# Kernel optimization log

Measured on AMD Instinct MI355X. Metric: run time of the kernel, lower is better.

Reference implementation:

```python
import jax, jax.numpy as jnp
import numpy as np

B, C, H, W = 8, 192, 128, 128
NH = 4  # num_heads
EPS = 1e-12


def setup_inputs() -> dict:
    key = jax.random.key(0)
    ks = jax.random.split(key, 10)
    s = 1.0 / np.sqrt(C)
    return {
        "x_q": jax.random.normal(ks[0], (B, C, H, W), jnp.float32),
        "x_k": jax.random.normal(ks[1], (B, C, H, W), jnp.float32),
        "Wq": jax.random.uniform(ks[2], (C, C), jnp.float32, -s, s),
        "bq": jax.random.uniform(ks[3], (C,), jnp.float32, -s, s),
        "Wkv": jax.random.uniform(ks[4], (2 * C, C), jnp.float32, -s, s),
        "bkv": jax.random.uniform(ks[5], (2 * C,), jnp.float32, -s, s),
        "Wp": jax.random.uniform(ks[6], (C, C), jnp.float32, -s, s),
        "bp": jax.random.uniform(ks[7], (C,), jnp.float32, -s, s),
        "temperature": jnp.ones((NH, 1, 1), jnp.float32),
    }


def _l2norm(x, axis):
    # torch F.normalize: x / clamp_min(||x||, eps)
    n = jnp.sqrt(jnp.sum(x * x, axis=axis, keepdims=True))
    return x / jnp.maximum(n, EPS)


def reference(x_q, x_k, Wq, bq, Wkv, bkv, Wp, bp, temperature):
    # 1x1 convs == channel matmuls
    q = jnp.einsum('oc,bchw->bohw', Wq, x_q) + bq[:, None, None]
    kv = jnp.einsum('oc,bchw->bohw', Wkv, x_k) + bkv[:, None, None]
    k, v = jnp.split(kv, 2, axis=1)

    def heads(t):  # (B,C,H,W) -> (B,NH,C//NH, H*W)
        return t.reshape(B, NH, C // NH, H * W)

    q, k, v = heads(q), heads(k), heads(v)
    q = _l2norm(q, 2)
    k = _l2norm(k, 2)

    attn_scale = 0.1 * jax.nn.sigmoid(temperature)  # (NH,1,1)
    attn = jnp.einsum('bhcd,bhkd->bhck', q, k) * attn_scale
    attn = jax.nn.softmax(attn, axis=-1)
    out = jnp.einsum('bhck,bhkd->bhcd', attn, v)
    out = out.reshape(B, C, H, W)
    out = jnp.einsum('oc,bchw->bohw', Wp, out) + bp[:, None, None]
    return out
```

## Files before the change

### kernel.cpp

```cpp
#include <hip/hip_runtime.h>
#include <hip/hip_bf16.h>

#define HW 16384
#define CC 192
#define BB 8
#define NHD 4
#define HD 48

typedef __attribute__((ext_vector_type(8))) short  short8;
typedef __attribute__((ext_vector_type(4))) float  f32x4;

static __device__ __forceinline__ unsigned short f2bf(float f) {
  unsigned u = __float_as_uint(f);
  u += 0x7fffu + ((u >> 16) & 1u);
  return (unsigned short)(u >> 16);
}
static __device__ __forceinline__ unsigned pk2bf(float lo, float hi) {
  __hip_bfloat162 h = __float22bfloat162_rn(make_float2(lo, hi));
  return *reinterpret_cast<unsigned*>(&h);
}

static __device__ __forceinline__ void ldsbar() {
  asm volatile("" ::: "memory");
  asm volatile("s_waitcnt lgkmcnt(0)" ::: "memory");
  __builtin_amdgcn_s_barrier();
  asm volatile("" ::: "memory");
}

#define SWZ_COL(row, cdw) ((cdw) ^ ((((row) >> 3) & 3) << 2))

__global__ __launch_bounds__(256) void cast_w_kernel(
    const float* __restrict__ Wq, const float* __restrict__ Wkv,
    unsigned short* __restrict__ Wb)
{
  const int i = blockIdx.x * 256 + threadIdx.x;
  const float v = (i < CC*CC) ? Wq[i] : Wkv[i - CC*CC];
  Wb[i] = f2bf(v);
}

__global__ __launch_bounds__(512, 2) void qkg_kernel(
    const float* __restrict__ x_q, const float* __restrict__ x_k,
    const unsigned short* __restrict__ wb,
    const float* __restrict__ bq, const float* __restrict__ bkv,
    float* __restrict__ gpart)
{
  const int tid  = threadIdx.x;
  const int lane = tid & 63;
  const int wv   = tid >> 6;
  const int half = wv >> 2;
  const int hh   = wv & 3;
  const int b    = blockIdx.y;
  const int p0   = blockIdx.x * 512;
  const int l15  = lane & 15;
  const int lg   = lane >> 4;
  const int ht   = tid & 255;
  const int qd   = ht & 15;

  __shared__ unsigned short Xsq[64][200];
  __shared__ unsigned short Xsk[64][200];
  __shared__ unsigned short QN[NHD][48][68];
  __shared__ unsigned short KN[NHD][48][68];

  const float* Xsrc = (half ? x_k : x_q) + (size_t)b*CC*HW;
  unsigned short (*Xdst)[200] = half ? Xsk : Xsq;
  unsigned short (*DST)[68]   = half ? KN[hh] : QN[hh];

  const unsigned short* W = wb + (size_t)half*CC*CC;
  short8 afr[6][3];
  #pragma unroll
  for (int kk = 0; kk < 6; ++kk)
    #pragma unroll
    for (int mt = 0; mt < 3; ++mt)
      afr[kk][mt] = *(const short8*)(W + (size_t)(hh*48 + mt*16 + l15)*CC + kk*32 + lg*8);

  const float* bias = half ? bkv : bq;
  float bv[3][4];
  #pragma unroll
  for (int mt = 0; mt < 3; ++mt)
    #pragma unroll
    for (int r = 0; r < 4; ++r)
      bv[mt][r] = bias[hh*48 + mt*16 + lg*4 + r];

  f32x4 pre[12];
  auto LOADT = [&](int pb) {
    #pragma unroll
    for (int i = 0; i < 6; ++i) {
      const int cp = (ht >> 4) + i*16;
      const float* base = Xsrc + (size_t)(2*cp)*HW + pb + qd*4;
      pre[2*i]   = *(const f32x4*)(base);
      pre[2*i+1] = *(const f32x4*)(base + HW);
    }
  };
  auto WRITET = [&]() {
    #pragma unroll
    for (int i = 0; i < 6; ++i) {
      const int cp = (ht >> 4) + i*16;
      #pragma unroll
      for (int j = 0; j < 4; ++j) {
        const int row = qd*4 + j;
        *(unsigned*)&Xdst[row][2*SWZ_COL(row, cp)] =
            pk2bf(pre[2*i][j], pre[2*i+1][j]);
      }
    }
  };

  f32x4 gacc[3][3];
  #pragma unroll
  for (int mt = 0; mt < 3; ++mt)
    #pragma unroll
    for (int nt = 0; nt < 3; ++nt)
      gacc[mt][nt] = (f32x4){0.f, 0.f, 0.f, 0.f};

  LOADT(p0);
  for (int t = 0; t < 8; ++t) {
    WRITET();
    ldsbar();
    if (t < 7) LOADT(p0 + (t+1)*64);

    f32x4 acc[3][4];
    #pragma unroll
    for (int mt = 0; mt < 3; ++mt)
      #pragma unroll
      for (int nt = 0; nt < 4; ++nt)
        acc[mt][nt] = (f32x4){0.f, 0.f, 0.f, 0.f};

    #pragma unroll
    for (int kk = 0; kk < 6; ++kk) {
      short8 bfr[4];
      #pragma unroll
      for (int nt = 0; nt < 4; ++nt) {
        const int lgs = lg ^ ((2*nt + (l15 >> 3)) & 3);
        bfr[nt] = *(const short8*)&Xdst[nt*16 + l15][kk*32 + lgs*8];
      }
      #pragma unroll
      for (int mt = 0; mt < 3; ++mt)
        #pragma unroll
        for (int nt = 0; nt < 4; ++nt)
          acc[mt][nt] = __builtin_amdgcn_mfma_f32_16x16x32_bf16(
              afr[kk][mt], bfr[nt], acc[mt][nt], 0, 0, 0);
    }

    #pragma unroll
    for (int nt = 0; nt < 4; ++nt) {
      float v[3][4];
      float ss = 0.f;
      #pragma unroll
      for (int mt = 0; mt < 3; ++mt)
        #pragma unroll
        for (int r = 0; r < 4; ++r) {
          const float x = acc[mt][nt][r] + bv[mt][r];
          v[mt][r] = x;
          ss += x*x;
        }
      ss += __shfl_xor(ss, 16);
      ss += __shfl_xor(ss, 32);
      const float rn = 1.0f / fmaxf(sqrtf(ss), 1e-12f);
      #pragma unroll
      for (int mt = 0; mt < 3; ++mt)
        #pragma unroll
        for (int r = 0; r < 4; ++r)
          DST[mt*16 + lg*4 + r][nt*16 + l15] = f2bf(v[mt][r] * rn);
    }
    ldsbar();

    {
      const int s = half;
      short8 ga[3], gb[3];
      #pragma unroll
      for (int mt = 0; mt < 3; ++mt)
        ga[mt] = *(const short8*)&QN[hh][mt*16 + l15][s*32 + lg*8];
      #pragma unroll
      for (int nt = 0; nt < 3; ++nt)
        gb[nt] = *(const short8*)&KN[hh][nt*16 + l15][s*32 + lg*8];
      #pragma unroll
      for (int mt = 0; mt < 3; ++mt)
        #pragma unroll
        for (int nt = 0; nt < 3; ++nt)
          gacc[mt][nt] = __builtin_amdgcn_mfma_f32_16x16x32_bf16(
              ga[mt], gb[nt], gacc[mt][nt], 0, 0, 0);
    }
  }

  float* G = gpart + ((size_t)(b*NHD + hh)*64 + blockIdx.x*2 + half)*2304;
  #pragma unroll
  for (int mt = 0; mt < 3; ++mt)
    #pragma unroll
    for (int nt = 0; nt < 3; ++nt)
      #pragma unroll
      for (int r = 0; r < 4; ++r)
        G[(mt*16 + lg*4 + r)*HD + nt*16 + l15] = gacc[mt][nt][r];
}

__global__ __launch_bounds__(256) void proj_fin(
    const float* __restrict__ x_k,
    const unsigned short* __restrict__ w3b,
    const float* __restrict__ b3,
    float* __restrict__ of)
{
  const int tid  = threadIdx.x;
  const int lane = tid & 63;
  const int wv   = tid >> 6;
  const int b    = blockIdx.y;
  const int p0   = blockIdx.x * 256;
  const int l15  = lane & 15;
  const int lg   = lane >> 4;
  const int qd   = tid & 15;

  __shared__ unsigned short Xt[2][64][200];

  const float* X = x_k + (size_t)b*CC*HW;
  const unsigned short* Wb = w3b + (size_t)b*CC*CC;
  const float* bias = b3 + (size_t)b*CC;

  short8 afr[6][3];
  #pragma unroll
  for (int kk = 0; kk < 6; ++kk)
    #pragma unroll
    for (int mt = 0; mt < 3; ++mt)
      afr[kk][mt] = *(const short8*)(Wb + (size_t)(wv*48 + mt*16 + l15)*CC + kk*32 + lg*8);

  float bv[3][4];
  #pragma unroll
  for (int mt = 0; mt < 3; ++mt)
    #pragma unroll
    for (int r = 0; r < 4; ++r)
      bv[mt][r] = bias[wv*48 + mt*16 + lg*4 + r];

  f32x4 pre[12];
  auto LOADT = [&](int pb) {
    #pragma unroll
    for (int i = 0; i < 6; ++i) {
      const int cp = (tid >> 4) + i*16;
      const float* base = X + (size_t)(2*cp)*HW + pb + qd*4;
      pre[2*i]   = *(const f32x4*)(base);
      pre[2*i+1] = *(const f32x4*)(base + HW);
    }
  };
  auto WRITET = [&](int buf) {
    #pragma unroll
    for (int i = 0; i < 6; ++i) {
      const int cp = (tid >> 4) + i*16;
      #pragma unroll
      for (int j = 0; j < 4; ++j) {
        const int row = qd*4 + j;
        *(unsigned*)&Xt[buf][row][2*SWZ_COL(row, cp)] =
            pk2bf(pre[2*i][j], pre[2*i+1][j]);
      }
    }
  };

  float* Ofp = of + (size_t)b*CC*HW;

  auto COMPUTE = [&](int buf, int pb) {
    f32x4 acc[3][4];
    #pragma unroll
    for (int mt = 0; mt < 3; ++mt)
      #pragma unroll
      for (int nt = 0; nt < 4; ++nt)
        acc[mt][nt] = (f32x4){0.f, 0.f, 0.f, 0.f};

    #pragma unroll
    for (int kk = 0; kk < 6; ++kk) {
      short8 bfr[4];
      #pragma unroll
      for (int nt = 0; nt < 4; ++nt) {
        const int lgs = lg ^ ((2*nt + (l15 >> 3)) & 3);
        bfr[nt] = *(const short8*)&Xt[buf][nt*16 + l15][kk*32 + lgs*8];
      }
      #pragma unroll
      for (int mt = 0; mt < 3; ++mt)
        #pragma unroll
        for (int nt = 0; nt < 4; ++nt)
          acc[mt][nt] = __builtin_amdgcn_mfma_f32_16x16x32_bf16(
              afr[kk][mt], bfr[nt], acc[mt][nt], 0, 0, 0);
    }

    #pragma unroll
    for (int nt = 0; nt < 4; ++nt) {
      const int col = pb + nt*16 + l15;
      #pragma unroll
      for (int mt = 0; mt < 3; ++mt)
        #pragma unroll
        for (int r = 0; r < 4; ++r)
          Ofp[(size_t)(wv*48 + mt*16 + lg*4 + r)*HW + col] = acc[mt][nt][r] + bv[mt][r];
    }
  };

  LOADT(p0);
  WRITET(0);
  ldsbar();
  #pragma unroll
  for (int t = 0; t < 4; ++t) {
    if (t < 3) LOADT(p0 + (t+1)*64);
    COMPUTE(t & 1, p0 + t*64);
    if (t < 3) {
      WRITET((t & 1) ^ 1);
      ldsbar();
    }
  }
}

__global__ __launch_bounds__(256) void attn_m_kernel(
    const float* __restrict__ Gpart,
    const float* __restrict__ Wp,
    const float* __restrict__ temp,
    float* __restrict__ Mf)
{
  __shared__ float att[HD][52];
  const int bh  = blockIdx.x;
  const int b   = bh >> 2, h = bh & 3;
  const int tid = threadIdx.x;
  const float* src = Gpart + (size_t)bh*64*2304;

  #pragma unroll
  for (int i = 0; i < 9; ++i) {
    const int e = tid + i*256;
    float s = 0.f;
    #pragma unroll
    for (int k = 0; k < 64; ++k) s += src[(size_t)k*2304 + e];
    att[e/48][e%48] = s;
  }
  __syncthreads();

  const int g = tid >> 2, sl = tid & 3;
  if (g < HD) {
    const float t = temp[h];
    const float scale = 0.1f / (1.0f + expf(-t));
    float* row = att[g];
    float m = -1e30f;
    #pragma unroll
    for (int jj = 0; jj < 12; ++jj) m = fmaxf(m, row[sl + jj*4]);
    m = fmaxf(m, __shfl_xor(m, 1));
    m = fmaxf(m, __shfl_xor(m, 2));
    float ev[12];
    float s = 0.f;
    #pragma unroll
    for (int jj = 0; jj < 12; ++jj) {
      const float e = expf((row[sl + jj*4] - m) * scale);
      ev[jj] = e; s += e;
    }
    s += __shfl_xor(s, 1);
    s += __shfl_xor(s, 2);
    const float inv = 1.0f / s;
    #pragma unroll
    for (int jj = 0; jj < 12; ++jj) row[sl + jj*4] = ev[jj] * inv;
  }
  __syncthreads();

  #pragma unroll
  for (int i = 0; i < 36; ++i) {
    const int idx = tid + i*256;
    const int o = idx / HD, k2 = idx % HD;
    const float* wrow = Wp + (size_t)o*CC + h*HD;
    float s = 0.f;
    #pragma unroll
    for (int c = 0; c < HD; ++c) s += wrow[c] * att[c][k2];
    Mf[(size_t)b*CC*CC + (size_t)o*CC + h*HD + k2] = s;
  }
}

__global__ __launch_bounds__(192) void w3_kernel(
    const float* __restrict__ Mf, const float* __restrict__ Wkv,
    const float* __restrict__ bkv, const float* __restrict__ bp,
    unsigned short* __restrict__ W3b, float* __restrict__ b3)
{
  const int b  = blockIdx.x;
  const int o0 = blockIdx.y * 8;
  const int j  = threadIdx.x;
  const float* M  = Mf + ((size_t)b*CC + o0)*CC;
  const float* Wv = Wkv + (size_t)CC*CC;
  const float* bv = bkv + CC;

  float acc[8]  = {0.f,0.f,0.f,0.f,0.f,0.f,0.f,0.f};
  float bacc[8] = {0.f,0.f,0.f,0.f,0.f,0.f,0.f,0.f};
  #pragma unroll 4
  for (int k = 0; k < CC; ++k) {
    const float w  = Wv[(size_t)k*CC + j];
    const float bk = bv[k];
    #pragma unroll
    for (int r = 0; r < 8; ++r) {
      const float m = M[r*CC + k];
      acc[r]  += m * w;
      bacc[r] += m * bk;
    }
  }
  unsigned short* dst = W3b + ((size_t)b*CC + o0)*CC + j;
  #pragma unroll
  for (int r = 0; r < 8; ++r) dst[(size_t)r*CC] = f2bf(acc[r]);
  if (j < 8) b3[(size_t)b*CC + o0 + j] = bacc[j] + bp[o0 + j];
}

extern "C" void kernel_launch(void* const* d_in, const int* in_sizes, int n_in,
                              void* d_out, int out_size, void* d_ws, size_t ws_size,
                              hipStream_t stream)
{
  (void)in_sizes; (void)n_in; (void)out_size; (void)ws_size;
  const float* x_q  = (const float*)d_in[0];
  const float* x_k  = (const float*)d_in[1];
  const float* Wq   = (const float*)d_in[2];
  const float* bq   = (const float*)d_in[3];
  const float* Wkv  = (const float*)d_in[4];
  const float* bkv  = (const float*)d_in[5];
  const float* Wp   = (const float*)d_in[6];
  const float* bp   = (const float*)d_in[7];
  const float* temp = (const float*)d_in[8];

  char* p = (char*)d_ws;
  float* gpart = (float*)p;                 p += (size_t)BB*NHD*64*2304*sizeof(float);
  float* mf = (float*)p;                    p += (size_t)BB*CC*CC*sizeof(float);
  unsigned short* w3b = (unsigned short*)p; p += (size_t)BB*CC*CC*sizeof(unsigned short);
  float* b3 = (float*)p;                    p += (size_t)BB*CC*sizeof(float);
  unsigned short* wb = (unsigned short*)p;

  cast_w_kernel<<<dim3((2*CC*CC)/256), 256, 0, stream>>>(Wq, Wkv, wb);

  qkg_kernel<<<dim3(HW/512, BB), 512, 0, stream>>>(
      x_q, x_k, wb, bq, bkv, gpart);

  attn_m_kernel<<<dim3(BB*NHD), 256, 0, stream>>>(gpart, Wp, temp, mf);
  w3_kernel<<<dim3(BB, 24), 192, 0, stream>>>(mf, Wkv, bkv, bp, w3b, b3);

  proj_fin<<<dim3(HW/256, BB), 256, 0, stream>>>(x_k, w3b, b3, (float*)d_out);
}
```

Baseline: 173.2 us.

## Alias normalized Q/K tiles onto X staging LDS and stream weight fragments

In the QK Gram kernel, the normalized Q/K tiles now reuse the X staging buffers instead of separate shared arrays, which lowers LDS per block. An extra barrier is added before the overwrite and at the end of each iteration to keep the aliasing safe. Both kernels now reload weight fragments from global memory per k-step instead of holding all 18 fragments in registers, and proj_fin gets a launch bound of 3 blocks per CU. The aim is higher occupancy from fewer registers and less LDS, at the cost of repeated weight loads and more synchronization.

```diff
diff --git a/kernel.cpp b/kernel.cpp
--- a/kernel.cpp
+++ b/kernel.cpp
@@ -56,23 +56,16 @@
   const int ht   = tid & 255;
   const int qd   = ht & 15;
 
-  __shared__ unsigned short Xsq[64][200];
-  __shared__ unsigned short Xsk[64][200];
-  __shared__ unsigned short QN[NHD][48][68];
-  __shared__ unsigned short KN[NHD][48][68];
+  __shared__ unsigned short LDS0[64][200];
+  __shared__ unsigned short LDS1[64][200];
+  unsigned short* QNb = &LDS0[0][0];
+  unsigned short* KNb = &LDS1[0][0];
 
   const float* Xsrc = (half ? x_k : x_q) + (size_t)b*CC*HW;
-  unsigned short (*Xdst)[200] = half ? Xsk : Xsq;
-  unsigned short (*DST)[68]   = half ? KN[hh] : QN[hh];
+  unsigned short (*Xdst)[200] = half ? LDS1 : LDS0;
+  unsigned short* DSTb = (half ? KNb : QNb) + hh*48*66;
 
   const unsigned short* W = wb + (size_t)half*CC*CC;
-  short8 afr[6][3];
-  #pragma unroll
-  for (int kk = 0; kk < 6; ++kk)
-    #pragma unroll
-    for (int mt = 0; mt < 3; ++mt)
-      afr[kk][mt] = *(const short8*)(W + (size_t)(hh*48 + mt*16 + l15)*CC + kk*32 + lg*8);
-
   const float* bias = half ? bkv : bq;
   float bv[3][4];
   #pragma unroll
@@ -126,7 +119,10 @@
 
     #pragma unroll
     for (int kk = 0; kk < 6; ++kk) {
-      short8 bfr[4];
+      short8 afr[3], bfr[4];
+      #pragma unroll
+      for (int mt = 0; mt < 3; ++mt)
+        afr[mt] = *(const short8*)(W + (size_t)(hh*48 + mt*16 + l15)*CC + kk*32 + lg*8);
       #pragma unroll
       for (int nt = 0; nt < 4; ++nt) {
         const int lgs = lg ^ ((2*nt + (l15 >> 3)) & 3);
@@ -137,19 +133,18 @@
         #pragma unroll
         for (int nt = 0; nt < 4; ++nt)
           acc[mt][nt] = __builtin_amdgcn_mfma_f32_16x16x32_bf16(
-              afr[kk][mt], bfr[nt], acc[mt][nt], 0, 0, 0);
+              afr[mt], bfr[nt], acc[mt][nt], 0, 0, 0);
     }
 
     #pragma unroll
     for (int nt = 0; nt < 4; ++nt) {
-      float v[3][4];
       float ss = 0.f;
       #pragma unroll
       for (int mt = 0; mt < 3; ++mt)
         #pragma unroll
         for (int r = 0; r < 4; ++r) {
           const float x = acc[mt][nt][r] + bv[mt][r];
-          v[mt][r] = x;
+          acc[mt][nt][r] = x;
           ss += x*x;
         }
       ss += __shfl_xor(ss, 16);
@@ -159,8 +154,17 @@
       for (int mt = 0; mt < 3; ++mt)
         #pragma unroll
         for (int r = 0; r < 4; ++r)
-          DST[mt*16 + lg*4 + r][nt*16 + l15] = f2bf(v[mt][r] * rn);
-    }
+          acc[mt][nt][r] *= rn;
+    }
+    ldsbar();
+
+    #pragma unroll
+    for (int nt = 0; nt < 4; ++nt)
+      #pragma unroll
+      for (int mt = 0; mt < 3; ++mt)
+        #pragma unroll
+        for (int r = 0; r < 4; ++r)
+          DSTb[(mt*16 + lg*4 + r)*66 + nt*16 + l15] = f2bf(acc[mt][nt][r]);
     ldsbar();
 
     {
@@ -168,10 +172,10 @@
       short8 ga[3], gb[3];
       #pragma unroll
       for (int mt = 0; mt < 3; ++mt)
-        ga[mt] = *(const short8*)&QN[hh][mt*16 + l15][s*32 + lg*8];
+        ga[mt] = *(const short8*)(QNb + hh*48*66 + (mt*16 + l15)*66 + s*32 + lg*8);
       #pragma unroll
       for (int nt = 0; nt < 3; ++nt)
-        gb[nt] = *(const short8*)&KN[hh][nt*16 + l15][s*32 + lg*8];
+        gb[nt] = *(const short8*)(KNb + hh*48*66 + (nt*16 + l15)*66 + s*32 + lg*8);
       #pragma unroll
       for (int mt = 0; mt < 3; ++mt)
         #pragma unroll
@@ -179,6 +183,7 @@
           gacc[mt][nt] = __builtin_amdgcn_mfma_f32_16x16x32_bf16(
               ga[mt], gb[nt], gacc[mt][nt], 0, 0, 0);
     }
+    ldsbar();
   }
 
   float* G = gpart + ((size_t)(b*NHD + hh)*64 + blockIdx.x*2 + half)*2304;
@@ -191,7 +196,7 @@
         G[(mt*16 + lg*4 + r)*HD + nt*16 + l15] = gacc[mt][nt][r];
 }
 
-__global__ __launch_bounds__(256) void proj_fin(
+__global__ __launch_bounds__(256, 3) void proj_fin(
     const float* __restrict__ x_k,
     const unsigned short* __restrict__ w3b,
     const float* __restrict__ b3,
@@ -212,13 +217,6 @@
   const unsigned short* Wb = w3b + (size_t)b*CC*CC;
   const float* bias = b3 + (size_t)b*CC;
 
-  short8 afr[6][3];
-  #pragma unroll
-  for (int kk = 0; kk < 6; ++kk)
-    #pragma unroll
-    for (int mt = 0; mt < 3; ++mt)
-      afr[kk][mt] = *(const short8*)(Wb + (size_t)(wv*48 + mt*16 + l15)*CC + kk*32 + lg*8);
-
   float bv[3][4];
   #pragma unroll
   for (int mt = 0; mt < 3; ++mt)
@@ -261,7 +259,10 @@
 
     #pragma unroll
     for (int kk = 0; kk < 6; ++kk) {
-      short8 bfr[4];
+      short8 afr[3], bfr[4];
+      #pragma unroll
+      for (int mt = 0; mt < 3; ++mt)
+        afr[mt] = *(const short8*)(Wb + (size_t)(wv*48 + mt*16 + l15)*CC + kk*32 + lg*8);
       #pragma unroll
       for (int nt = 0; nt < 4; ++nt) {
         const int lgs = lg ^ ((2*nt + (l15 >> 3)) & 3);
@@ -272,7 +273,7 @@
         #pragma unroll
         for (int nt = 0; nt < 4; ++nt)
           acc[mt][nt] = __builtin_amdgcn_mfma_f32_16x16x32_bf16(
-              afr[kk][mt], bfr[nt], acc[mt][nt], 0, 0, 0);
+              afr[mt], bfr[nt], acc[mt][nt], 0, 0, 0);
     }
 
     #pragma unroll
```

After: 212.2 us. 22.5% more time.

## Load 128-pixel rows per wave, write LDS in alternating halves, reload weights per k-step

Applied to the files above, without the earlier changes.

The X-tile global loads are reorganized so each wave reads 48 channels across 128 contiguous pixels, refilling every other iteration. Half the lanes write their 64-pixel slice to LDS on alternate iterations, using a new XOR swizzle and 16-bit scattered stores. The weight A-fragments are no longer kept resident in registers and are reloaded from global/L2 for each k-step. This frees registers and lengthens contiguous global reads, at the cost of repeated weight loads, narrower LDS stores and possible bank conflicts.

```diff
diff --git a/kernel.cpp b/kernel.cpp
--- a/kernel.cpp
+++ b/kernel.cpp
@@ -27,6 +27,8 @@
   asm volatile("" ::: "memory");
 }
 
+#define SWZ3(rowq) ((((rowq) & 7)) << 3)
+
 #define SWZ_COL(row, cdw) ((cdw) ^ ((((row) >> 3) & 3) << 2))
 
 __global__ __launch_bounds__(256) void cast_w_kernel(
@@ -49,12 +51,13 @@
   const int wv   = tid >> 6;
   const int half = wv >> 2;
   const int hh   = wv & 3;
+  const int wq   = wv & 3;
   const int b    = blockIdx.y;
   const int p0   = blockIdx.x * 512;
   const int l15  = lane & 15;
   const int lg   = lane >> 4;
-  const int ht   = tid & 255;
-  const int qd   = ht & 15;
+  const int ch2  = lane >> 5;
+  const int pl32 = lane & 31;
 
   __shared__ unsigned short Xsq[64][200];
   __shared__ unsigned short Xsk[64][200];
@@ -66,13 +69,6 @@
   unsigned short (*DST)[68]   = half ? KN[hh] : QN[hh];
 
   const unsigned short* W = wb + (size_t)half*CC*CC;
-  short8 afr[6][3];
-  #pragma unroll
-  for (int kk = 0; kk < 6; ++kk)
-    #pragma unroll
-    for (int mt = 0; mt < 3; ++mt)
-      afr[kk][mt] = *(const short8*)(W + (size_t)(hh*48 + mt*16 + l15)*CC + kk*32 + lg*8);
-
   const float* bias = half ? bkv : bq;
   float bv[3][4];
   #pragma unroll
@@ -81,25 +77,27 @@
     for (int r = 0; r < 4; ++r)
       bv[mt][r] = bias[hh*48 + mt*16 + lg*4 + r];
 
-  f32x4 pre[12];
-  auto LOADT = [&](int pb) {
-    #pragma unroll
-    for (int i = 0; i < 6; ++i) {
-      const int cp = (ht >> 4) + i*16;
-      const float* base = Xsrc + (size_t)(2*cp)*HW + pb + qd*4;
-      pre[2*i]   = *(const f32x4*)(base);
-      pre[2*i+1] = *(const f32x4*)(base + HW);
+  f32x4 pre[24];
+  auto LOADT = [&](int pbase) {
+    #pragma unroll
+    for (int i = 0; i < 24; ++i) {
+      const int c = wq*48 + 2*i + ch2;
+      pre[i] = *(const f32x4*)(Xsrc + (size_t)c*HW + pbase + pl32*4);
     }
   };
-  auto WRITET = [&]() {
-    #pragma unroll
-    for (int i = 0; i < 6; ++i) {
-      const int cp = (ht >> 4) + i*16;
-      #pragma unroll
-      for (int j = 0; j < 4; ++j) {
-        const int row = qd*4 + j;
-        *(unsigned*)&Xdst[row][2*SWZ_COL(row, cp)] =
-            pk2bf(pre[2*i][j], pre[2*i+1][j]);
+  auto WRITET = [&](int sel) {
+    if ((pl32 >> 4) == sel) {
+      const int pq = pl32 & 15;
+      #pragma unroll
+      for (int i = 0; i < 24; ++i) {
+        const int c  = wq*48 + 2*i + ch2;
+        const int cs = c ^ SWZ3(pq);
+        const unsigned u0 = pk2bf(pre[i][0], pre[i][1]);
+        const unsigned u1 = pk2bf(pre[i][2], pre[i][3]);
+        Xdst[pq*4 + 0][cs] = (unsigned short)u0;
+        Xdst[pq*4 + 1][cs] = (unsigned short)(u0 >> 16);
+        Xdst[pq*4 + 2][cs] = (unsigned short)u1;
+        Xdst[pq*4 + 3][cs] = (unsigned short)(u1 >> 16);
       }
     }
   };
@@ -113,9 +111,9 @@
 
   LOADT(p0);
   for (int t = 0; t < 8; ++t) {
-    WRITET();
+    WRITET(t & 1);
     ldsbar();
-    if (t < 7) LOADT(p0 + (t+1)*64);
+    if ((t & 1) && t < 7) LOADT(p0 + (t+1)*64);
 
     f32x4 acc[3][4];
     #pragma unroll
@@ -126,18 +124,21 @@
 
     #pragma unroll
     for (int kk = 0; kk < 6; ++kk) {
-      short8 bfr[4];
+      short8 afr[3], bfr[4];
+      #pragma unroll
+      for (int mt = 0; mt < 3; ++mt)
+        afr[mt] = *(const short8*)(W + (size_t)(hh*48 + mt*16 + l15)*CC + kk*32 + lg*8);
       #pragma unroll
       for (int nt = 0; nt < 4; ++nt) {
-        const int lgs = lg ^ ((2*nt + (l15 >> 3)) & 3);
-        bfr[nt] = *(const short8*)&Xdst[nt*16 + l15][kk*32 + lgs*8];
+        const int rowq = (nt*16 + l15) >> 2;
+        bfr[nt] = *(const short8*)&Xdst[nt*16 + l15][(kk*32 + lg*8) ^ SWZ3(rowq)];
       }
       #pragma unroll
       for (int mt = 0; mt < 3; ++mt)
         #pragma unroll
         for (int nt = 0; nt < 4; ++nt)
           acc[mt][nt] = __builtin_amdgcn_mfma_f32_16x16x32_bf16(
-              afr[kk][mt], bfr[nt], acc[mt][nt], 0, 0, 0);
+              afr[mt], bfr[nt], acc[mt][nt], 0, 0, 0);
     }
 
     #pragma unroll
```

Result: slower. 273.8 us (+58.1%).
